# Kernel optimization log

Measured on AMD Instinct MI355X. Metric: run time of the kernel, lower is better.

The kernel has to match this reference:

```python
import jax, jax.numpy as jnp
import numpy as np

NS, NG, NV = 16, 8, 8          # scalar, gate, vector(l=1) multiplicities
CIN = 8                        # input irreps: 8x0
COUT1 = NS + NG + 3 * NV       # 48 channels into gate
CMID = NS + 3 * NV             # 40 channels after gate
KS = 3                         # kernel size
NB = 4                         # radial basis count
P = KS ** 3
BN_EPS = 1e-5

EPS3 = (jnp.zeros((3, 3, 3))
        .at[0, 1, 2].set(1.).at[1, 2, 0].set(1.).at[2, 0, 1].set(1.)
        .at[0, 2, 1].set(-1.).at[2, 1, 0].set(-1.).at[1, 0, 2].set(-1.))


def _lattice():
    c = jnp.linspace(-1., 1., KS)
    g = jnp.stack(jnp.meshgrid(c, c, c, indexing='ij'), -1).reshape(-1, 3)  # [P,3]
    r = jnp.linalg.norm(g, axis=-1)
    rhat = jnp.where(r[:, None] > 0., g / jnp.maximum(r, 1e-9)[:, None], 0.)
    sh0 = jnp.ones_like(r)             # Y_0, component normalization
    sh1 = jnp.sqrt(3.) * rhat          # Y_1, component normalization
    # soft_one_hot_linspace(r, 0, 1, NB, 'smooth_finite', cutoff=False)
    centers = jnp.linspace(0., 1., NB)
    step = centers[1] - centers[0]
    d = (r[:, None] - centers[None, :]) / step
    emb = jnp.where(jnp.abs(d) < 1.,
                    1.14136 * jnp.exp(2.) * jnp.exp(-1. / jnp.maximum(1. - d ** 2, 1e-9)),
                    0.)
    return sh0, sh1, emb


def _kernel1(w1, emb, sh0, sh1):
    # per-lattice-point tensor-product weights: 8x0 (x) (0+1) -> 16x0 + 8x0 + 8x1
    W = (emb @ w1) / KS ** 1.5                 # [P, 256]
    w_ss = W[:, :128].reshape(P, CIN, NS)
    w_sg = W[:, 128:192].reshape(P, CIN, NG)
    w_sv = W[:, 192:256].reshape(P, CIN, NV)
    a = 1. / jnp.sqrt(8.)                      # fan-in per output irrep
    Km = jnp.zeros((P, CIN, COUT1))
    Km = Km.at[:, :, :NS].set(a * w_ss * sh0[:, None, None])
    Km = Km.at[:, :, NS:NS + NG].set(a * w_sg * sh0[:, None, None])
    kv = a * jnp.einsum('pij,pm->pijm', w_sv, sh1)
    return Km.at[:, :, NS + NG:].set(kv.reshape(P, CIN, 3 * NV))


def _kernel2(w2, emb, sh0, sh1):
    # (16x0 + 8x1) (x) (0+1) -> 16x0 + 8x0 + 8x1 with l<=1 CG paths
    W = (emb @ w2) / KS ** 1.5                 # [P, 832]
    w_ss = W[:, 0:256].reshape(P, NS, NS)
    w_sg = W[:, 256:384].reshape(P, NS, NG)
    w_sv = W[:, 384:512].reshape(P, NS, NV)
    w_vv0 = W[:, 512:576].reshape(P, NV, NV)
    w_vs = W[:, 576:704].reshape(P, NV, NS)
    w_vg = W[:, 704:768].reshape(P, NV, NG)
    w_vv1 = W[:, 768:832].reshape(P, NV, NV)
    a_s = 1. / jnp.sqrt(16. + 8.)
    a_v = 1. / jnp.sqrt(16. + 8. + 8.)
    Km = jnp.zeros((P, CMID, COUT1))
    Km = Km.at[:, :NS, :NS].set(a_s * w_ss * sh0[:, None, None])
    Km = Km.at[:, :NS, NS:NS + NG].set(a_s * w_sg * sh0[:, None, None])
    Km = Km.at[:, :NS, NS + NG:].set(
        (a_v * jnp.einsum('pij,pm->pijm', w_sv, sh1)).reshape(P, NS, 3 * NV))
    ks = (a_s / jnp.sqrt(3.)) * jnp.einsum('puj,pm->pumj', w_vs, sh1)
    kg = (a_s / jnp.sqrt(3.)) * jnp.einsum('puj,pm->pumj', w_vg, sh1)
    kv0 = a_v * jnp.einsum('puj,p,mn->pumjn', w_vv0, sh0, jnp.eye(3))
    kv1 = (a_v / jnp.sqrt(6.)) * jnp.einsum('puj,msn,ps->pumjn', w_vv1, EPS3, sh1)
    Km = Km.at[:, NS:, :NS].set(ks.reshape(P, 3 * NV, NS))
    Km = Km.at[:, NS:, NS:NS + NG].set(kg.reshape(P, 3 * NV, NG))
    return Km.at[:, NS:, NS + NG:].set((kv0 + kv1).reshape(P, 3 * NV, 3 * NV))


def _conv3d(x, Km, cin):
    ker = Km.reshape(KS, KS, KS, cin, COUT1).transpose(4, 3, 0, 1, 2)  # [O,I,k,k,k]
    return jax.lax.conv_general_dilated(
        x, ker, (1, 1, 1), 'SAME',
        dimension_numbers=('NCDHW', 'OIDHW', 'NCDHW'))


def _batchnorm(x, ws, bs, wv):
    # e3nn BatchNorm, training statistics, reduce='mean'; x channel-last [...,48]
    s = x[..., :NS + NG]
    mu = s.mean(axis=(0, 1, 2, 3))
    s = s - mu
    var = (s ** 2).mean(axis=(0, 1, 2, 3))
    s = s / jnp.sqrt(var + BN_EPS) * ws + bs
    v = x[..., NS + NG:].reshape(x.shape[:-1] + (NV, 3))
    n2 = (v ** 2).sum(-1).mean(axis=(0, 1, 2, 3))   # [NV]
    v = v * (((n2 + BN_EPS) ** -0.5) * wv)[:, None]
    return jnp.concatenate([s, v.reshape(x.shape[:-1] + (3 * NV,))], -1)


def _gate(x):
    # Gate: relu on scalars, sigmoid gates multiply l=1 fields
    s = jax.nn.relu(x[..., :NS])
    g = jax.nn.sigmoid(x[..., NS:NS + NG])
    v = x[..., NS + NG:].reshape(x.shape[:-1] + (NV, 3)) * g[..., None]
    return jnp.concatenate([s, v.reshape(x.shape[:-1] + (3 * NV,))], -1)


def _forward(x, w1, sc1, w2, sc2_s, sc2_v,
             bn1_ws, bn1_bs, bn1_wv, bn2_ws, bn2_bs, bn2_wv):
    sh0, sh1, emb = _lattice()
    y = _conv3d(x, _kernel1(w1, emb, sh0, sh1), CIN)
    y = y.at[:, :NS + NG].add(
        jnp.einsum('bixyz,io->boxyz', x, sc1) / jnp.sqrt(8.))  # self-connection
    y = jnp.moveaxis(y, 1, -1)
    y = _gate(_batchnorm(y, bn1_ws, bn1_bs, bn1_wv))           # dropout p=0: identity
    y = jnp.moveaxis(y, -1, 1)                                 # [B, 40, X, Y, Z]
    z = _conv3d(y, _kernel2(w2, emb, sh0, sh1), CMID)
    z = z.at[:, :NS + NG].add(
        jnp.einsum('bixyz,io->boxyz', y[:, :NS], sc2_s) / jnp.sqrt(16.))
    yv = y[:, NS:].reshape(y.shape[0], NV, 3, *y.shape[2:])
    scv = jnp.einsum('bumxyz,uj->bjmxyz', yv, sc2_v) / jnp.sqrt(8.)
    z = z.at[:, NS + NG:].add(scv.reshape(z.shape[0], 3 * NV, *z.shape[2:]))
    z = jnp.moveaxis(z, 1, -1)
    z = _gate(_batchnorm(z, bn2_ws, bn2_bs, bn2_wv))
    return jnp.moveaxis(z, -1, 1)                              # [B, 40, X, Y, Z]


def setup_inputs() -> dict:
    key = jax.random.key(0)
    ks = jax.random.split(key, 8)
    B, S = 1, 64
    return {
        'x': jax.random.normal(ks[0], (B, CIN, S, S, S), jnp.float32),
        'w1': jax.random.normal(ks[1], (NB, 256), jnp.float32),
        'sc1': jax.random.normal(ks[2], (CIN, NS + NG), jnp.float32),
        'w2': jax.random.normal(ks[3], (NB, 832), jnp.float32),
        'sc2_s': jax.random.normal(ks[4], (NS, NS + NG), jnp.float32),
        'sc2_v': jax.random.normal(ks[5], (NV, NV), jnp.float32),
        'bn1_ws': jnp.ones((NS + NG,), jnp.float32),
        'bn1_bs': jnp.zeros((NS + NG,), jnp.float32),
        'bn1_wv': jnp.ones((NV,), jnp.float32),
        'bn2_ws': jnp.ones((NS + NG,), jnp.float32),
        'bn2_bs': jnp.zeros((NS + NG,), jnp.float32),
        'bn2_wv': jnp.ones((NV,), jnp.float32),
    }


def reference(x, w1, sc1, w2, sc2_s, sc2_v,
              bn1_ws, bn1_bs, bn1_wv, bn2_ws, bn2_bs, bn2_wv):
    return _forward(x, w1, sc1, w2, sc2_s, sc2_v,
                    bn1_ws, bn1_bs, bn1_wv, bn2_ws, bn2_bs, bn2_wv)
```

## Files before the change

kernel.cpp:

```cpp
#include <hip/hip_runtime.h>
#include <math.h>

#define N3 262144


#define TBL_TOTAL 1728

__device__ inline void lattice_emb(int p, float* embr) {
    int i = p / 9, j = (p / 3) % 3, k = p % 3;
    float gx = (float)(i - 1), gy = (float)(j - 1), gz = (float)(k - 1);
    float r = sqrtf(gx * gx + gy * gy + gz * gz);
    const float centers[4] = {0.f, 0.33333334f, 0.6666667f, 1.f};
    const float step = 0.33333334f;
    #pragma unroll
    for (int b = 0; b < 4; b++) {
        float dd = (r - centers[b]) / step;
        float e = 0.f;
        if (fabsf(dd) < 1.f)
            e = 1.14136f * expf(2.f) * expf(-1.f / fmaxf(1.f - dd * dd, 1e-9f));
        embr[b] = e;
    }
}

__global__ __launch_bounds__(256) void build_tables_kernel(
        const float* __restrict__ w1,  const float* __restrict__ sc1,
        const float* __restrict__ w2,  const float* __restrict__ sc2s,
        const float* __restrict__ sc2v, float* __restrict__ T,
        float* __restrict__ stats1, float* __restrict__ stats2) {
    int gid = blockIdx.x * 256 + threadIdx.x;
    if (gid >= TBL_TOTAL) {
        int r = gid - TBL_TOTAL;
        if (r < 72) stats1[r] = 0.f;
        else if (r < 144) stats2[r - 72] = 0.f;
        return;
    }

    const float inv_ks15 = 0.19245008972987526f;
    const float s3   = 1.7320508075688772f;
    const float a1   = 0.35355339059327373f;
    const float a_s  = 0.2041241452319315f;
    const float a_v  = 0.17677669529663687f;
    const float a_s3 = 0.11785113019775793f;
    const float a_v6 = 0.07216878364870322f;

    float embC[4], embF[4];
    lattice_emb(13, embC);
    lattice_emb(22, embF);

    auto WC1 = [&](int c) { float s=0.f;
        #pragma unroll
        for (int b=0;b<4;b++) s += embC[b]*w1[b*256+c]; return s*inv_ks15; };
    auto WF1 = [&](int c) { float s=0.f;
        #pragma unroll
        for (int b=0;b<4;b++) s += embF[b]*w1[b*256+c]; return s*inv_ks15; };
    auto WC2 = [&](int c) { float s=0.f;
        #pragma unroll
        for (int b=0;b<4;b++) s += embC[b]*w2[b*832+c]; return s*inv_ks15; };
    auto WF2 = [&](int c) { float s=0.f;
        #pragma unroll
        for (int b=0;b<4;b++) s += embF[b]*w2[b*832+c]; return s*inv_ks15; };

    float val = 0.f;
    if (gid < 192) {
        int i = gid / 24, o = gid % 24;
        int c = (o < 16) ? i * 16 + o : 128 + i * 8 + (o - 16);
        val = a1 * WC1(c) + a1 * sc1[i * 24 + o];
    } else if (gid < 384) {
        int r = gid - 192; int i = r / 24, o = r % 24;
        int c = (o < 16) ? i * 16 + o : 128 + i * 8 + (o - 16);
        val = a1 * WF1(c);
    } else if (gid < 448) {
        int r = gid - 384; int i = r / 8, jj = r % 8;
        val = a1 * s3 * WF1(192 + i * 8 + jj);
    } else if (gid < 832) {
        int r = gid - 448; int i = r / 24, o = r % 24;
        int c = (o < 16) ? i * 16 + o : 256 + i * 8 + (o - 16);
        val = a_s * WC2(c) + 0.25f * sc2s[i * 24 + o];
    } else if (gid < 1216) {
        int r = gid - 832; int i = r / 24, o = r % 24;
        int c = (o < 16) ? i * 16 + o : 256 + i * 8 + (o - 16);
        val = a_s * WF2(c);
    } else if (gid < 1344) {
        int r = gid - 1216; int i = r / 8, jj = r % 8;
        val = a_v * s3 * WF2(384 + i * 8 + jj);
    } else if (gid < 1536) {
        int r = gid - 1344; int u = r / 24, o = r % 24;
        int c = (o < 16) ? 576 + u * 16 + o : 704 + u * 8 + (o - 16);
        val = a_s3 * s3 * WF2(c);
    } else if (gid < 1600) {
        int r = gid - 1536; int u = r / 8, jj = r % 8;
        val = a_v * WC2(512 + u * 8 + jj) + a1 * sc2v[u * 8 + jj];
    } else if (gid < 1664) {
        int r = gid - 1600; int u = r / 8, jj = r % 8;
        val = a_v * WF2(512 + u * 8 + jj);
    } else {
        int r = gid - 1664; int u = r / 8, jj = r % 8;
        val = a_v6 * s3 * WF2(768 + u * 8 + jj);
    }
    T[gid] = val;
}

__device__ inline float4 f4z() { return make_float4(0.f, 0.f, 0.f, 0.f); }
__device__ inline float4 f4add(float4 a, float4 b) {
    return make_float4(a.x+b.x, a.y+b.y, a.z+b.z, a.w+b.w); }
__device__ inline float4 f4sub(float4 a, float4 b) {
    return make_float4(a.x-b.x, a.y-b.y, a.z-b.z, a.w-b.w); }
__device__ inline float4 f4fma(float s, float4 a, float4 c) {
    return make_float4(fmaf(s,a.x,c.x), fmaf(s,a.y,c.y), fmaf(s,a.z,c.z), fmaf(s,a.w,c.w)); }
__device__ inline float f4sum(float4 a) { return a.x+a.y+a.z+a.w; }
__device__ inline float f4dot(float4 a) { return a.x*a.x+a.y*a.y+a.z*a.z+a.w*a.w; }

#define LQ5(BP, C_, DM_, DP_, HM_, HP_)                                       \
    {                                                                         \
        const float* _p = (BP);                                               \
        C_  = *(const float4*)_p;                                             \
        DM_ = dmok ? *(const float4*)(_p - 4096) : f4z();                     \
        DP_ = dpok ? *(const float4*)(_p + 4096) : f4z();                     \
        HM_ = hmok ? *(const float4*)(_p -   64) : f4z();                     \
        HP_ = hpok ? *(const float4*)(_p +   64) : f4z();                     \
    }

#define WQ(C_, WM_, WP_)                                                      \
    {                                                                         \
        float _lw = __shfl_up((C_).w, 1, 64);                                 \
        float _rw = __shfl_down((C_).x, 1, 64);                               \
        WM_ = make_float4(wL ? 0.f : _lw, (C_).x, (C_).y, (C_).z);            \
        WP_ = make_float4((C_).y, (C_).z, (C_).w, wR ? 0.f : _rw);            \
    }

__global__ __launch_bounds__(256, 2) void conv1_kernel(const float* __restrict__ x,
                                                       const float* __restrict__ Tg,
                                                       float* __restrict__ out,
                                                       float* __restrict__ stats) {
    __shared__ float T[448];
    __shared__ float red[4][48];
    for (int t = threadIdx.x; t < 448; t += 256) T[t] = Tg[t];
    __syncthreads();

    const int ohalf = blockIdx.y;
    int idx = blockIdx.x * 1024 + threadIdx.x * 4;
    int w0 = idx & 63, h = (idx >> 6) & 63, d = idx >> 12;
    bool dmok = d > 0, dpok = d < 63, hmok = h > 0, hpok = h < 63;
    bool wL = (w0 == 0), wR = (w0 == 60);

    float4 acc[24];
    #pragma unroll
    for (int o = 0; o < 24; o++) acc[o] = f4z();

    float4 nc, ndm, ndp, nhm, nhp;
    LQ5(x + idx, nc, ndm, ndp, nhm, nhp);

    if (ohalf == 0) {
        #pragma unroll 1
        for (int i = 0; i < 8; i++) {
            float4 c = nc, dmq = ndm, dpq = ndp, hmq = nhm, hpq = nhp;
            if (i < 7) LQ5(x + (i + 1) * N3 + idx, nc, ndm, ndp, nhm, nhp);
            float4 wmq, wpq; WQ(c, wmq, wpq);
            float4 S = f4add(f4add(f4add(dmq, dpq), f4add(hmq, hpq)), f4add(wmq, wpq));
            const float* tc = &T[i * 24];
            const float* tf = &T[192 + i * 24];
            #pragma unroll
            for (int o = 0; o < 24; o++)
                acc[o] = f4fma(tc[o], c, f4fma(tf[o], S, acc[o]));
        }
    } else {
        #pragma unroll 1
        for (int i = 0; i < 8; i++) {
            float4 c = nc, dmq = ndm, dpq = ndp, hmq = nhm, hpq = nhp;
            if (i < 7) LQ5(x + (i + 1) * N3 + idx, nc, ndm, ndp, nhm, nhp);
            float4 wmq, wpq; WQ(c, wmq, wpq);
            float4 Dd = f4sub(dpq, dmq), Dh = f4sub(hpq, hmq), Dw = f4sub(wpq, wmq);
            const float* tv = &T[384 + i * 8];
            #pragma unroll
            for (int jj = 0; jj < 8; jj++) {
                float wv = tv[jj];
                acc[jj * 3 + 0] = f4fma(wv, Dd, acc[jj * 3 + 0]);
                acc[jj * 3 + 1] = f4fma(wv, Dh, acc[jj * 3 + 1]);
                acc[jj * 3 + 2] = f4fma(wv, Dw, acc[jj * 3 + 2]);
            }
        }
    }

    int obase = ohalf * 24;
    #pragma unroll
    for (int o = 0; o < 24; o++)
        *(float4*)(out + (obase + o) * N3 + idx) = acc[o];

    int lane = threadIdx.x & 63, wvx = threadIdx.x >> 6;
    if (ohalf == 0) {
        #pragma unroll
        for (int q = 0; q < 48; q++) {
            float val = (q < 24) ? f4sum(acc[q]) : f4dot(acc[q - 24]);
            #pragma unroll
            for (int mq = 32; mq >= 1; mq >>= 1) val += __shfl_xor(val, mq, 64);
            if (lane == 0) red[wvx][q] = val;
        }
        __syncthreads();
        if (threadIdx.x < 48)
            atomicAdd(&stats[threadIdx.x],
                      red[0][threadIdx.x] + red[1][threadIdx.x] +
                      red[2][threadIdx.x] + red[3][threadIdx.x]);
    } else {
        #pragma unroll
        for (int q = 0; q < 24; q++) {
            float val = f4dot(acc[q]);
            #pragma unroll
            for (int mq = 32; mq >= 1; mq >>= 1) val += __shfl_xor(val, mq, 64);
            if (lane == 0) red[wvx][q] = val;
        }
        __syncthreads();
        if (threadIdx.x < 24)
            atomicAdd(&stats[48 + threadIdx.x],
                      red[0][threadIdx.x] + red[1][threadIdx.x] +
                      red[2][threadIdx.x] + red[3][threadIdx.x]);
    }
}

__global__ __launch_bounds__(256, 2) void conv2_kernel(const float* __restrict__ y,
                                                       const float* __restrict__ Tg,
                                                       float* __restrict__ out,
                                                       float* __restrict__ stats) {
    __shared__ float T[1280];
    __shared__ float red[4][48];
    for (int t = threadIdx.x; t < 1280; t += 256) T[t] = Tg[448 + t];
    __syncthreads();

    const int ohalf = blockIdx.y;
    int idx = blockIdx.x * 1024 + threadIdx.x * 4;
    int w0 = idx & 63, h = (idx >> 6) & 63, d = idx >> 12;
    bool dmok = d > 0, dpok = d < 63, hmok = h > 0, hpok = h < 63;
    bool wL = (w0 == 0), wR = (w0 == 60);

    float4 acc[24];
    #pragma unroll
    for (int o = 0; o < 24; o++) acc[o] = f4z();

    if (ohalf == 0) {
        float4 nc, ndm, ndp, nhm, nhp;
        LQ5(y + idx, nc, ndm, ndp, nhm, nhp);
        #pragma unroll 1
        for (int i = 0; i < 16; i++) {
            float4 c = nc, dmq = ndm, dpq = ndp, hmq = nhm, hpq = nhp;
            if (i < 15) LQ5(y + (i + 1) * N3 + idx, nc, ndm, ndp, nhm, nhp);
            float4 wmq, wpq; WQ(c, wmq, wpq);
            float4 S = f4add(f4add(f4add(dmq, dpq), f4add(hmq, hpq)), f4add(wmq, wpq));
            const float* tc = &T[i * 24];
            const float* tf = &T[384 + i * 24];
            #pragma unroll
            for (int o = 0; o < 24; o++)
                acc[o] = f4fma(tc[o], c, f4fma(tf[o], S, acc[o]));
        }
        #pragma unroll 1
        for (int u = 0; u < 8; u++) {
            const float* b0 = y + (16 + u * 3) * N3 + idx;
            float4 qdm = dmok ? *(const float4*)(b0 - 4096) : f4z();
            float4 qdp = dpok ? *(const float4*)(b0 + 4096) : f4z();
            float4 qhm = hmok ? *(const float4*)(b0 + N3 - 64) : f4z();
            float4 qhp = hpok ? *(const float4*)(b0 + N3 + 64) : f4z();
            float4 c2  = *(const float4*)(b0 + 2 * N3);
            float4 wmq, wpq; WQ(c2, wmq, wpq);
            float4 Dsum = f4add(f4add(f4sub(qdp, qdm), f4sub(qhp, qhm)), f4sub(wpq, wmq));
            const float* tvs = &T[896 + u * 24];
            #pragma unroll
            for (int o = 0; o < 24; o++)
                acc[o] = f4fma(tvs[o], Dsum, acc[o]);
        }
    } else {
        float4 nc, ndm, ndp, nhm, nhp;
        LQ5(y + idx, nc, ndm, ndp, nhm, nhp);
        #pragma unroll 1
        for (int i = 0; i < 16; i++) {
            float4 c = nc, dmq = ndm, dpq = ndp, hmq = nhm, hpq = nhp;
            if (i < 15) LQ5(y + (i + 1) * N3 + idx, nc, ndm, ndp, nhm, nhp);
            float4 wmq, wpq; WQ(c, wmq, wpq);
            float4 Dd = f4sub(dpq, dmq), Dh = f4sub(hpq, hmq), Dw = f4sub(wpq, wmq);
            const float* tv = &T[768 + i * 8];
            #pragma unroll
            for (int jj = 0; jj < 8; jj++) {
                float wv = tv[jj];
                acc[jj * 3 + 0] = f4fma(wv, Dd, acc[jj * 3 + 0]);
                acc[jj * 3 + 1] = f4fma(wv, Dh, acc[jj * 3 + 1]);
                acc[jj * 3 + 2] = f4fma(wv, Dw, acc[jj * 3 + 2]);
            }
        }
        #pragma unroll 1
        for (int u = 0; u < 8; u++) {
            const float* t0c = &T[1088 + u * 8];
            const float* t0f = &T[1152 + u * 8];
            const float* tv1 = &T[1216 + u * 8];
            {
                float4 c, dmq, dpq, hmq, hpq;
                LQ5(y + (16 + u * 3 + 0) * N3 + idx, c, dmq, dpq, hmq, hpq);
                float4 wmq, wpq; WQ(c, wmq, wpq);
                float4 S = f4add(f4add(f4add(dmq, dpq), f4add(hmq, hpq)), f4add(wmq, wpq));
                float4 Dh = f4sub(hpq, hmq), Dw = f4sub(wpq, wmq);
                #pragma unroll
                for (int jj = 0; jj < 8; jj++) {
                    float k1 = tv1[jj];
                    acc[jj * 3 + 0] = f4fma(t0c[jj], c, f4fma(t0f[jj], S, acc[jj * 3 + 0]));
                    acc[jj * 3 + 2] = f4fma(k1, Dh, acc[jj * 3 + 2]);
                    acc[jj * 3 + 1] = f4fma(-k1, Dw, acc[jj * 3 + 1]);
                }
            }
            {
                float4 c, dmq, dpq, hmq, hpq;
                LQ5(y + (16 + u * 3 + 1) * N3 + idx, c, dmq, dpq, hmq, hpq);
                float4 wmq, wpq; WQ(c, wmq, wpq);
                float4 S = f4add(f4add(f4add(dmq, dpq), f4add(hmq, hpq)), f4add(wmq, wpq));
                float4 Dd = f4sub(dpq, dmq), Dw = f4sub(wpq, wmq);
                #pragma unroll
                for (int jj = 0; jj < 8; jj++) {
                    float k1 = tv1[jj];
                    acc[jj * 3 + 1] = f4fma(t0c[jj], c, f4fma(t0f[jj], S, acc[jj * 3 + 1]));
                    acc[jj * 3 + 0] = f4fma(k1, Dw, acc[jj * 3 + 0]);
                    acc[jj * 3 + 2] = f4fma(-k1, Dd, acc[jj * 3 + 2]);
                }
            }
            {
                float4 c, dmq, dpq, hmq, hpq;
                LQ5(y + (16 + u * 3 + 2) * N3 + idx, c, dmq, dpq, hmq, hpq);
                float4 wmq, wpq; WQ(c, wmq, wpq);
                float4 S = f4add(f4add(f4add(dmq, dpq), f4add(hmq, hpq)), f4add(wmq, wpq));
                float4 Dd = f4sub(dpq, dmq), Dh = f4sub(hpq, hmq);
                #pragma unroll
                for (int jj = 0; jj < 8; jj++) {
                    float k1 = tv1[jj];
                    acc[jj * 3 + 2] = f4fma(t0c[jj], c, f4fma(t0f[jj], S, acc[jj * 3 + 2]));
                    acc[jj * 3 + 1] = f4fma(k1, Dd, acc[jj * 3 + 1]);
                    acc[jj * 3 + 0] = f4fma(-k1, Dh, acc[jj * 3 + 0]);
                }
            }
        }
    }

    int obase = ohalf * 24;
    #pragma unroll
    for (int o = 0; o < 24; o++)
        *(float4*)(out + (obase + o) * N3 + idx) = acc[o];

    int lane = threadIdx.x & 63, wvx = threadIdx.x >> 6;
    if (ohalf == 0) {
        #pragma unroll
        for (int q = 0; q < 48; q++) {
            float val = (q < 24) ? f4sum(acc[q]) : f4dot(acc[q - 24]);
            #pragma unroll
            for (int mq = 32; mq >= 1; mq >>= 1) val += __shfl_xor(val, mq, 64);
            if (lane == 0) red[wvx][q] = val;
        }
        __syncthreads();
        if (threadIdx.x < 48)
            atomicAdd(&stats[threadIdx.x],
                      red[0][threadIdx.x] + red[1][threadIdx.x] +
                      red[2][threadIdx.x] + red[3][threadIdx.x]);
    } else {
        #pragma unroll
        for (int q = 0; q < 24; q++) {
            float val = f4dot(acc[q]);
            #pragma unroll
            for (int mq = 32; mq >= 1; mq >>= 1) val += __shfl_xor(val, mq, 64);
            if (lane == 0) red[wvx][q] = val;
        }
        __syncthreads();
        if (threadIdx.x < 24)
            atomicAdd(&stats[48 + threadIdx.x],
                      red[0][threadIdx.x] + red[1][threadIdx.x] +
                      red[2][threadIdx.x] + red[3][threadIdx.x]);
    }
}

__global__ __launch_bounds__(256) void bn_gate_kernel(const float* __restrict__ zp,
                                                      const float* __restrict__ stats,
                                                      const float* __restrict__ wsc,
                                                      const float* __restrict__ bsc,
                                                      const float* __restrict__ wvc,
                                                      float* __restrict__ out) {
    __shared__ float sb[56];
    if (threadIdx.x < 32) {
        int t = threadIdx.x;
        const float invN = 1.0f / 262144.0f;
        if (t < 24) {
            float mu = stats[t] * invN;
            float var = stats[24 + t] * invN - mu * mu;
            float inv = rsqrtf(var + 1e-5f);
            sb[t] = wsc[t] * inv;
            sb[24 + t] = bsc[t] - mu * wsc[t] * inv;
        } else {
            int u = t - 24;
            float s2 = stats[48 + u * 3] + stats[48 + u * 3 + 1] + stats[48 + u * 3 + 2];
            sb[48 + u] = wvc[u] * rsqrtf(s2 * invN + 1e-5f);
        }
    }
    __syncthreads();

    int idx = (blockIdx.x * 256 + threadIdx.x) * 2;
    float2 g[8];
    #pragma unroll
    for (int u = 0; u < 8; u++) {
        float2 v = *(const float2*)(zp + (16 + u) * N3 + idx);
        float sc = sb[16 + u], bi = sb[40 + u];
        g[u].x = 1.0f / (1.0f + expf(-(v.x * sc + bi)));
        g[u].y = 1.0f / (1.0f + expf(-(v.y * sc + bi)));
    }
    #pragma unroll
    for (int c = 0; c < 16; c++) {
        float2 v = *(const float2*)(zp + c * N3 + idx);
        float sc = sb[c], bi = sb[24 + c];
        float2 r;
        r.x = fmaxf(v.x * sc + bi, 0.f);
        r.y = fmaxf(v.y * sc + bi, 0.f);
        *(float2*)(out + c * N3 + idx) = r;
    }
    #pragma unroll
    for (int u = 0; u < 8; u++) {
        float sv = sb[48 + u];
        #pragma unroll
        for (int m = 0; m < 3; m++) {
            float2 v = *(const float2*)(zp + (24 + u * 3 + m) * N3 + idx);
            float2 r;
            r.x = v.x * sv * g[u].x;
            r.y = v.y * sv * g[u].y;
            *(float2*)(out + (16 + u * 3 + m) * N3 + idx) = r;
        }
    }
}

extern "C" void kernel_launch(void* const* d_in, const int* in_sizes, int n_in,
                              void* d_out, int out_size, void* d_ws, size_t ws_size,
                              hipStream_t stream) {
    const float* x      = (const float*)d_in[0];
    const float* w1     = (const float*)d_in[1];
    const float* sc1    = (const float*)d_in[2];
    const float* w2     = (const float*)d_in[3];
    const float* sc2s   = (const float*)d_in[4];
    const float* sc2v   = (const float*)d_in[5];
    const float* bn1_ws = (const float*)d_in[6];
    const float* bn1_bs = (const float*)d_in[7];
    const float* bn1_wv = (const float*)d_in[8];
    const float* bn2_ws = (const float*)d_in[9];
    const float* bn2_bs = (const float*)d_in[10];
    const float* bn2_wv = (const float*)d_in[11];
    float* out = (float*)d_out;
    char* ws = (char*)d_ws;

    float* Tg     = (float*)(ws + 0);
    float* stats1 = (float*)(ws + 8192);
    float* stats2 = (float*)(ws + 8192 + 512);
    float* bufA   = (float*)(ws + 262144);

    hipLaunchKernelGGL(build_tables_kernel, dim3(8), dim3(256), 0, stream,
                       w1, sc1, w2, sc2s, sc2v, Tg, stats1, stats2);
    hipLaunchKernelGGL(conv1_kernel, dim3(256, 2), dim3(256), 0, stream, x, Tg, bufA, stats1);
    hipLaunchKernelGGL(bn_gate_kernel, dim3(512), dim3(256), 0, stream,
                       bufA, stats1, bn1_ws, bn1_bs, bn1_wv, out);
    hipLaunchKernelGGL(conv2_kernel, dim3(256, 2), dim3(256), 0, stream, out, Tg, bufA, stats2);
    hipLaunchKernelGGL(bn_gate_kernel, dim3(512), dim3(256), 0, stream,
                       bufA, stats2, bn2_ws, bn2_bs, bn2_wv, out);
}
```

Measured before the change: 111.1 us.

## Fuse conv and BN-gate stages via cooperative grid sync, keep accumulators in registers

Each convolution is merged with its batch-norm and gate step into one cooperative kernel. After accumulating, each block publishes its channel statistics, waits at a grid-wide barrier, then applies normalization, ReLU and sigmoid gating straight from its register accumulators. Only the 8 gate channels go through a scratch buffer, because the vector-half blocks need them. This removes the round trip of the full 48-channel pre-normalization tensor through global memory and drops two kernel launches. In exchange it adds a grid barrier and depends on all 512 blocks being resident at once, with a fallback to the old separate kernels if the cooperative launch fails.

```diff
diff --git a/kernel.cpp b/kernel.cpp
--- a/kernel.cpp
+++ b/kernel.cpp
@@ -1,5 +1,8 @@
 #include <hip/hip_runtime.h>
+#include <hip/hip_cooperative_groups.h>
 #include <math.h>
+
+namespace cg = cooperative_groups;
 
 #define N3 262144
 
@@ -109,6 +112,7 @@
     return make_float4(fmaf(s,a.x,c.x), fmaf(s,a.y,c.y), fmaf(s,a.z,c.z), fmaf(s,a.w,c.w)); }
 __device__ inline float f4sum(float4 a) { return a.x+a.y+a.z+a.w; }
 __device__ inline float f4dot(float4 a) { return a.x*a.x+a.y*a.y+a.z*a.z+a.w*a.w; }
+__device__ inline float sigm(float v) { return 1.0f / (1.0f + expf(-v)); }
 
 #define LQ5(BP, C_, DM_, DP_, HM_, HP_)                                       \
     {                                                                         \
@@ -128,244 +132,270 @@
         WP_ = make_float4((C_).y, (C_).z, (C_).w, wR ? 0.f : _rw);            \
     }
 
-__global__ __launch_bounds__(256, 2) void conv1_kernel(const float* __restrict__ x,
-                                                       const float* __restrict__ Tg,
-                                                       float* __restrict__ out,
-                                                       float* __restrict__ stats) {
+#define CONV1_BODY(SRC)                                                       \
+    {                                                                         \
+        float4 nc, ndm, ndp, nhm, nhp;                                        \
+        LQ5((SRC) + idx, nc, ndm, ndp, nhm, nhp);                             \
+        if (ohalf == 0) {                                                     \
+            _Pragma("unroll 1")                                               \
+            for (int i = 0; i < 8; i++) {                                     \
+                float4 c = nc, dmq = ndm, dpq = ndp, hmq = nhm, hpq = nhp;    \
+                if (i < 7) LQ5((SRC) + (i + 1) * N3 + idx, nc, ndm, ndp, nhm, nhp); \
+                float4 wmq, wpq; WQ(c, wmq, wpq);                             \
+                float4 S = f4add(f4add(f4add(dmq, dpq), f4add(hmq, hpq)), f4add(wmq, wpq)); \
+                const float* tc = &T[i * 24];                                 \
+                const float* tf = &T[192 + i * 24];                           \
+                _Pragma("unroll")                                             \
+                for (int o = 0; o < 24; o++)                                  \
+                    acc[o] = f4fma(tc[o], c, f4fma(tf[o], S, acc[o]));        \
+            }                                                                 \
+        } else {                                                              \
+            _Pragma("unroll 1")                                               \
+            for (int i = 0; i < 8; i++) {                                     \
+                float4 c = nc, dmq = ndm, dpq = ndp, hmq = nhm, hpq = nhp;    \
+                if (i < 7) LQ5((SRC) + (i + 1) * N3 + idx, nc, ndm, ndp, nhm, nhp); \
+                float4 wmq, wpq; WQ(c, wmq, wpq);                             \
+                float4 Dd = f4sub(dpq, dmq), Dh = f4sub(hpq, hmq), Dw = f4sub(wpq, wmq); \
+                const float* tv = &T[384 + i * 8];                            \
+                _Pragma("unroll")                                             \
+                for (int jj = 0; jj < 8; jj++) {                              \
+                    float wv = tv[jj];                                        \
+                    acc[jj * 3 + 0] = f4fma(wv, Dd, acc[jj * 3 + 0]);         \
+                    acc[jj * 3 + 1] = f4fma(wv, Dh, acc[jj * 3 + 1]);         \
+                    acc[jj * 3 + 2] = f4fma(wv, Dw, acc[jj * 3 + 2]);         \
+                }                                                             \
+            }                                                                 \
+        }                                                                     \
+    }
+
+#define CONV2_BODY(SRC)                                                       \
+    if (ohalf == 0) {                                                         \
+        float4 nc, ndm, ndp, nhm, nhp;                                        \
+        LQ5((SRC) + idx, nc, ndm, ndp, nhm, nhp);                             \
+        _Pragma("unroll 1")                                                   \
+        for (int i = 0; i < 16; i++) {                                        \
+            float4 c = nc, dmq = ndm, dpq = ndp, hmq = nhm, hpq = nhp;        \
+            if (i < 15) LQ5((SRC) + (i + 1) * N3 + idx, nc, ndm, ndp, nhm, nhp); \
+            float4 wmq, wpq; WQ(c, wmq, wpq);                                 \
+            float4 S = f4add(f4add(f4add(dmq, dpq), f4add(hmq, hpq)), f4add(wmq, wpq)); \
+            const float* tc = &T[i * 24];                                     \
+            const float* tf = &T[384 + i * 24];                               \
+            _Pragma("unroll")                                                 \
+            for (int o = 0; o < 24; o++)                                      \
+                acc[o] = f4fma(tc[o], c, f4fma(tf[o], S, acc[o]));            \
+        }                                                                     \
+        _Pragma("unroll 1")                                                   \
+        for (int u = 0; u < 8; u++) {                                         \
+            const float* b0 = (SRC) + (16 + u * 3) * N3 + idx;                \
+            float4 qdm = dmok ? *(const float4*)(b0 - 4096) : f4z();          \
+            float4 qdp = dpok ? *(const float4*)(b0 + 4096) : f4z();          \
+            float4 qhm = hmok ? *(const float4*)(b0 + N3 - 64) : f4z();       \
+            float4 qhp = hpok ? *(const float4*)(b0 + N3 + 64) : f4z();       \
+            float4 c2  = *(const float4*)(b0 + 2 * N3);                       \
+            float4 wmq, wpq; WQ(c2, wmq, wpq);                                \
+            float4 Dsum = f4add(f4add(f4sub(qdp, qdm), f4sub(qhp, qhm)), f4sub(wpq, wmq)); \
+            const float* tvs = &T[896 + u * 24];                              \
+            _Pragma("unroll")                                                 \
+            for (int o = 0; o < 24; o++)                                      \
+                acc[o] = f4fma(tvs[o], Dsum, acc[o]);                         \
+        }                                                                     \
+    } else {                                                                  \
+        float4 nc, ndm, ndp, nhm, nhp;                                        \
+        LQ5((SRC) + idx, nc, ndm, ndp, nhm, nhp);                             \
+        _Pragma("unroll 1")                                                   \
+        for (int i = 0; i < 16; i++) {                                        \
+            float4 c = nc, dmq = ndm, dpq = ndp, hmq = nhm, hpq = nhp;        \
+            if (i < 15) LQ5((SRC) + (i + 1) * N3 + idx, nc, ndm, ndp, nhm, nhp); \
+            float4 wmq, wpq; WQ(c, wmq, wpq);                                 \
+            float4 Dd = f4sub(dpq, dmq), Dh = f4sub(hpq, hmq), Dw = f4sub(wpq, wmq); \
+            const float* tv = &T[768 + i * 8];                                \
+            _Pragma("unroll")                                                 \
+            for (int jj = 0; jj < 8; jj++) {                                  \
+                float wv = tv[jj];                                            \
+                acc[jj * 3 + 0] = f4fma(wv, Dd, acc[jj * 3 + 0]);             \
+                acc[jj * 3 + 1] = f4fma(wv, Dh, acc[jj * 3 + 1]);             \
+                acc[jj * 3 + 2] = f4fma(wv, Dw, acc[jj * 3 + 2]);             \
+            }                                                                 \
+        }                                                                     \
+        _Pragma("unroll 1")                                                   \
+        for (int u = 0; u < 8; u++) {                                         \
+            const float* t0c = &T[1088 + u * 8];                              \
+            const float* t0f = &T[1152 + u * 8];                              \
+            const float* tv1 = &T[1216 + u * 8];                              \
+            {                                                                 \
+                float4 c, dmq, dpq, hmq, hpq;                                 \
+                LQ5((SRC) + (16 + u * 3 + 0) * N3 + idx, c, dmq, dpq, hmq, hpq); \
+                float4 wmq, wpq; WQ(c, wmq, wpq);                             \
+                float4 S = f4add(f4add(f4add(dmq, dpq), f4add(hmq, hpq)), f4add(wmq, wpq)); \
+                float4 Dh = f4sub(hpq, hmq), Dw = f4sub(wpq, wmq);            \
+                _Pragma("unroll")                                             \
+                for (int jj = 0; jj < 8; jj++) {                              \
+                    float k1 = tv1[jj];                                       \
+                    acc[jj * 3 + 0] = f4fma(t0c[jj], c, f4fma(t0f[jj], S, acc[jj * 3 + 0])); \
+                    acc[jj * 3 + 2] = f4fma(k1, Dh, acc[jj * 3 + 2]);         \
+                    acc[jj * 3 + 1] = f4fma(-k1, Dw, acc[jj * 3 + 1]);        \
+                }                                                             \
+            }                                                                 \
+            {                                                                 \
+                float4 c, dmq, dpq, hmq, hpq;                                 \
+                LQ5((SRC) + (16 + u * 3 + 1) * N3 + idx, c, dmq, dpq, hmq, hpq); \
+                float4 wmq, wpq; WQ(c, wmq, wpq);                             \
+                float4 S = f4add(f4add(f4add(dmq, dpq), f4add(hmq, hpq)), f4add(wmq, wpq)); \
+                float4 Dd = f4sub(dpq, dmq), Dw = f4sub(wpq, wmq);            \
+                _Pragma("unroll")                                             \
+                for (int jj = 0; jj < 8; jj++) {                              \
+                    float k1 = tv1[jj];                                       \
+                    acc[jj * 3 + 1] = f4fma(t0c[jj], c, f4fma(t0f[jj], S, acc[jj * 3 + 1])); \
+                    acc[jj * 3 + 0] = f4fma(k1, Dw, acc[jj * 3 + 0]);         \
+                    acc[jj * 3 + 2] = f4fma(-k1, Dd, acc[jj * 3 + 2]);        \
+                }                                                             \
+            }                                                                 \
+            {                                                                 \
+                float4 c, dmq, dpq, hmq, hpq;                                 \
+                LQ5((SRC) + (16 + u * 3 + 2) * N3 + idx, c, dmq, dpq, hmq, hpq); \
+                float4 wmq, wpq; WQ(c, wmq, wpq);                             \
+                float4 S = f4add(f4add(f4add(dmq, dpq), f4add(hmq, hpq)), f4add(wmq, wpq)); \
+                float4 Dd = f4sub(dpq, dmq), Dh = f4sub(hpq, hmq);            \
+                _Pragma("unroll")                                             \
+                for (int jj = 0; jj < 8; jj++) {                              \
+                    float k1 = tv1[jj];                                       \
+                    acc[jj * 3 + 2] = f4fma(t0c[jj], c, f4fma(t0f[jj], S, acc[jj * 3 + 2])); \
+                    acc[jj * 3 + 1] = f4fma(k1, Dd, acc[jj * 3 + 1]);         \
+                    acc[jj * 3 + 0] = f4fma(-k1, Dh, acc[jj * 3 + 0]);        \
+                }                                                             \
+            }                                                                 \
+        }                                                                     \
+    }
+
+#define STATS_REDUCE(STATS)                                                   \
+    {                                                                         \
+        int lane = threadIdx.x & 63, wvx = threadIdx.x >> 6;                  \
+        if (ohalf == 0) {                                                     \
+            _Pragma("unroll")                                                 \
+            for (int q = 0; q < 48; q++) {                                    \
+                float val = (q < 24) ? f4sum(acc[q]) : f4dot(acc[q - 24]);    \
+                _Pragma("unroll")                                             \
+                for (int mq = 32; mq >= 1; mq >>= 1) val += __shfl_xor(val, mq, 64); \
+                if (lane == 0) red[wvx][q] = val;                             \
+            }                                                                 \
+            __syncthreads();                                                  \
+            if (threadIdx.x < 48)                                             \
+                atomicAdd(&(STATS)[threadIdx.x],                              \
+                          red[0][threadIdx.x] + red[1][threadIdx.x] +         \
+                          red[2][threadIdx.x] + red[3][threadIdx.x]);         \
+        } else {                                                              \
+            _Pragma("unroll")                                                 \
+            for (int q = 0; q < 24; q++) {                                    \
+                float val = f4dot(acc[q]);                                    \
+                _Pragma("unroll")                                             \
+                for (int mq = 32; mq >= 1; mq >>= 1) val += __shfl_xor(val, mq, 64); \
+                if (lane == 0) red[wvx][q] = val;                             \
+            }                                                                 \
+            __syncthreads();                                                  \
+            if (threadIdx.x < 24)                                             \
+                atomicAdd(&(STATS)[48 + threadIdx.x],                         \
+                          red[0][threadIdx.x] + red[1][threadIdx.x] +         \
+                          red[2][threadIdx.x] + red[3][threadIdx.x]);         \
+        }                                                                     \
+    }
+
+#define FINALIZE_SB(STATS, WSC, BSC, WVC)                                     \
+    if (threadIdx.x < 32) {                                                   \
+        int t = threadIdx.x;                                                  \
+        const float invN = 1.0f / 262144.0f;                                  \
+        if (t < 24) {                                                         \
+            float mu = (STATS)[t] * invN;                                     \
+            float var = (STATS)[24 + t] * invN - mu * mu;                     \
+            float inv = rsqrtf(var + 1e-5f);                                  \
+            sb[t] = (WSC)[t] * inv;                                           \
+            sb[24 + t] = (BSC)[t] - mu * (WSC)[t] * inv;                      \
+        } else {                                                              \
+            int u = t - 24;                                                   \
+            float s2 = (STATS)[48 + u * 3] + (STATS)[48 + u * 3 + 1] +        \
+                       (STATS)[48 + u * 3 + 2];                               \
+            sb[48 + u] = (WVC)[u] * rsqrtf(s2 * invN + 1e-5f);                \
+        }                                                                     \
+    }                                                                         \
+    __syncthreads();
+
+#define GATED_EPILOGUE(DST, GBUF)                                             \
+    if (ohalf == 0) {                                                         \
+        _Pragma("unroll")                                                     \
+        for (int c = 0; c < 16; c++) {                                        \
+            float4 v = acc[c];                                                \
+            float scl = sb[c], bi = sb[24 + c];                               \
+            float4 r;                                                         \
+            r.x = fmaxf(v.x * scl + bi, 0.f);                                 \
+            r.y = fmaxf(v.y * scl + bi, 0.f);                                 \
+            r.z = fmaxf(v.z * scl + bi, 0.f);                                 \
+            r.w = fmaxf(v.w * scl + bi, 0.f);                                 \
+            *(float4*)((DST) + c * N3 + idx) = r;                             \
+        }                                                                     \
+    } else {                                                                  \
+        _Pragma("unroll 1")                                                   \
+        for (int u = 0; u < 8; u++) {                                         \
+            float4 gv = *(const float4*)((GBUF) + u * N3 + idx);              \
+            float scl = sb[16 + u], bi = sb[40 + u], sv = sb[48 + u];         \
+            float4 g;                                                         \
+            g.x = sigm(gv.x * scl + bi) * sv;                                 \
+            g.y = sigm(gv.y * scl + bi) * sv;                                 \
+            g.z = sigm(gv.z * scl + bi) * sv;                                 \
+            g.w = sigm(gv.w * scl + bi) * sv;                                 \
+            _Pragma("unroll")                                                 \
+            for (int m = 0; m < 3; m++) {                                     \
+                float4 a = acc[u * 3 + m];                                    \
+                float4 r = make_float4(a.x * g.x, a.y * g.y, a.z * g.z, a.w * g.w); \
+                *(float4*)((DST) + (16 + u * 3 + m) * N3 + idx) = r;          \
+            }                                                                 \
+        }                                                                     \
+    }
+
+__global__ __launch_bounds__(256, 2) void conv1_plain(const float* __restrict__ x,
+                                                      const float* __restrict__ Tg,
+                                                      float* __restrict__ out,
+                                                      float* __restrict__ stats) {
     __shared__ float T[448];
     __shared__ float red[4][48];
     for (int t = threadIdx.x; t < 448; t += 256) T[t] = Tg[t];
     __syncthreads();
-
     const int ohalf = blockIdx.y;
     int idx = blockIdx.x * 1024 + threadIdx.x * 4;
     int w0 = idx & 63, h = (idx >> 6) & 63, d = idx >> 12;
     bool dmok = d > 0, dpok = d < 63, hmok = h > 0, hpok = h < 63;
     bool wL = (w0 == 0), wR = (w0 == 60);
-
     float4 acc[24];
     #pragma unroll
     for (int o = 0; o < 24; o++) acc[o] = f4z();
-
-    float4 nc, ndm, ndp, nhm, nhp;
-    LQ5(x + idx, nc, ndm, ndp, nhm, nhp);
-
-    if (ohalf == 0) {
-        #pragma unroll 1
-        for (int i = 0; i < 8; i++) {
-            float4 c = nc, dmq = ndm, dpq = ndp, hmq = nhm, hpq = nhp;
-            if (i < 7) LQ5(x + (i + 1) * N3 + idx, nc, ndm, ndp, nhm, nhp);
-            float4 wmq, wpq; WQ(c, wmq, wpq);
-            float4 S = f4add(f4add(f4add(dmq, dpq), f4add(hmq, hpq)), f4add(wmq, wpq));
-            const float* tc = &T[i * 24];
-            const float* tf = &T[192 + i * 24];
-            #pragma unroll
-            for (int o = 0; o < 24; o++)
-                acc[o] = f4fma(tc[o], c, f4fma(tf[o], S, acc[o]));
-        }
-    } else {
-        #pragma unroll 1
-        for (int i = 0; i < 8; i++) {
-            float4 c = nc, dmq = ndm, dpq = ndp, hmq = nhm, hpq = nhp;
-            if (i < 7) LQ5(x + (i + 1) * N3 + idx, nc, ndm, ndp, nhm, nhp);
-            float4 wmq, wpq; WQ(c, wmq, wpq);
-            float4 Dd = f4sub(dpq, dmq), Dh = f4sub(hpq, hmq), Dw = f4sub(wpq, wmq);
-            const float* tv = &T[384 + i * 8];
-            #pragma unroll
-            for (int jj = 0; jj < 8; jj++) {
-                float wv = tv[jj];
-                acc[jj * 3 + 0] = f4fma(wv, Dd, acc[jj * 3 + 0]);
-                acc[jj * 3 + 1] = f4fma(wv, Dh, acc[jj * 3 + 1]);
-                acc[jj * 3 + 2] = f4fma(wv, Dw, acc[jj * 3 + 2]);
-            }
-        }
-    }
-
+    CONV1_BODY(x);
     int obase = ohalf * 24;
     #pragma unroll
     for (int o = 0; o < 24; o++)
         *(float4*)(out + (obase + o) * N3 + idx) = acc[o];
-
-    int lane = threadIdx.x & 63, wvx = threadIdx.x >> 6;
-    if (ohalf == 0) {
-        #pragma unroll
-        for (int q = 0; q < 48; q++) {
-            float val = (q < 24) ? f4sum(acc[q]) : f4dot(acc[q - 24]);
-            #pragma unroll
-            for (int mq = 32; mq >= 1; mq >>= 1) val += __shfl_xor(val, mq, 64);
-            if (lane == 0) red[wvx][q] = val;
-        }
-        __syncthreads();
-        if (threadIdx.x < 48)
-            atomicAdd(&stats[threadIdx.x],
-                      red[0][threadIdx.x] + red[1][threadIdx.x] +
-                      red[2][threadIdx.x] + red[3][threadIdx.x]);
-    } else {
-        #pragma unroll
-        for (int q = 0; q < 24; q++) {
-            float val = f4dot(acc[q]);
-            #pragma unroll
-            for (int mq = 32; mq >= 1; mq >>= 1) val += __shfl_xor(val, mq, 64);
-            if (lane == 0) red[wvx][q] = val;
-        }
-        __syncthreads();
-        if (threadIdx.x < 24)
-            atomicAdd(&stats[48 + threadIdx.x],
-                      red[0][threadIdx.x] + red[1][threadIdx.x] +
-                      red[2][threadIdx.x] + red[3][threadIdx.x]);
-    }
-}
-
-__global__ __launch_bounds__(256, 2) void conv2_kernel(const float* __restrict__ y,
-                                                       const float* __restrict__ Tg,
-                                                       float* __restrict__ out,
-                                                       float* __restrict__ stats) {
+    STATS_REDUCE(stats);
+}
+
+__global__ __launch_bounds__(256, 2) void conv2_plain(const float* __restrict__ y,
+                                                      const float* __restrict__ Tg,
+                                                      float* __restrict__ out,
+                                                      float* __restrict__ stats) {
     __shared__ float T[1280];
     __shared__ float red[4][48];
     for (int t = threadIdx.x; t < 1280; t += 256) T[t] = Tg[448 + t];
     __syncthreads();
-
     const int ohalf = blockIdx.y;
     int idx = blockIdx.x * 1024 + threadIdx.x * 4;
     int w0 = idx & 63, h = (idx >> 6) & 63, d = idx >> 12;
     bool dmok = d > 0, dpok = d < 63, hmok = h > 0, hpok = h < 63;
     bool wL = (w0 == 0), wR = (w0 == 60);
-
     float4 acc[24];
     #pragma unroll
     for (int o = 0; o < 24; o++) acc[o] = f4z();
-
-    if (ohalf == 0) {
-        float4 nc, ndm, ndp, nhm, nhp;
-        LQ5(y + idx, nc, ndm, ndp, nhm, nhp);
-        #pragma unroll 1
-        for (int i = 0; i < 16; i++) {
-            float4 c = nc, dmq = ndm, dpq = ndp, hmq = nhm, hpq = nhp;
-            if (i < 15) LQ5(y + (i + 1) * N3 + idx, nc, ndm, ndp, nhm, nhp);
-            float4 wmq, wpq; WQ(c, wmq, wpq);
-            float4 S = f4add(f4add(f4add(dmq, dpq), f4add(hmq, hpq)), f4add(wmq, wpq));
-            const float* tc = &T[i * 24];
-            const float* tf = &T[384 + i * 24];
-            #pragma unroll
-            for (int o = 0; o < 24; o++)
-                acc[o] = f4fma(tc[o], c, f4fma(tf[o], S, acc[o]));
-        }
-        #pragma unroll 1
-        for (int u = 0; u < 8; u++) {
-            const float* b0 = y + (16 + u * 3) * N3 + idx;
-            float4 qdm = dmok ? *(const float4*)(b0 - 4096) : f4z();
-            float4 qdp = dpok ? *(const float4*)(b0 + 4096) : f4z();
-            float4 qhm = hmok ? *(const float4*)(b0 + N3 - 64) : f4z();
-            float4 qhp = hpok ? *(const float4*)(b0 + N3 + 64) : f4z();
-            float4 c2  = *(const float4*)(b0 + 2 * N3);
-            float4 wmq, wpq; WQ(c2, wmq, wpq);
-            float4 Dsum = f4add(f4add(f4sub(qdp, qdm), f4sub(qhp, qhm)), f4sub(wpq, wmq));
-            const float* tvs = &T[896 + u * 24];
-            #pragma unroll
-            for (int o = 0; o < 24; o++)
-                acc[o] = f4fma(tvs[o], Dsum, acc[o]);
-        }
-    } else {
-        float4 nc, ndm, ndp, nhm, nhp;
-        LQ5(y + idx, nc, ndm, ndp, nhm, nhp);
-        #pragma unroll 1
-        for (int i = 0; i < 16; i++) {
-            float4 c = nc, dmq = ndm, dpq = ndp, hmq = nhm, hpq = nhp;
-            if (i < 15) LQ5(y + (i + 1) * N3 + idx, nc, ndm, ndp, nhm, nhp);
-            float4 wmq, wpq; WQ(c, wmq, wpq);
-            float4 Dd = f4sub(dpq, dmq), Dh = f4sub(hpq, hmq), Dw = f4sub(wpq, wmq);
-            const float* tv = &T[768 + i * 8];
-            #pragma unroll
-            for (int jj = 0; jj < 8; jj++) {
-                float wv = tv[jj];
-                acc[jj * 3 + 0] = f4fma(wv, Dd, acc[jj * 3 + 0]);
-                acc[jj * 3 + 1] = f4fma(wv, Dh, acc[jj * 3 + 1]);
-                acc[jj * 3 + 2] = f4fma(wv, Dw, acc[jj * 3 + 2]);
-            }
-        }
-        #pragma unroll 1
-        for (int u = 0; u < 8; u++) {
-            const float* t0c = &T[1088 + u * 8];
-            const float* t0f = &T[1152 + u * 8];
-            const float* tv1 = &T[1216 + u * 8];
-            {
-                float4 c, dmq, dpq, hmq, hpq;
-                LQ5(y + (16 + u * 3 + 0) * N3 + idx, c, dmq, dpq, hmq, hpq);
-                float4 wmq, wpq; WQ(c, wmq, wpq);
-                float4 S = f4add(f4add(f4add(dmq, dpq), f4add(hmq, hpq)), f4add(wmq, wpq));
-                float4 Dh = f4sub(hpq, hmq), Dw = f4sub(wpq, wmq);
-                #pragma unroll
-                for (int jj = 0; jj < 8; jj++) {
-                    float k1 = tv1[jj];
-                    acc[jj * 3 + 0] = f4fma(t0c[jj], c, f4fma(t0f[jj], S, acc[jj * 3 + 0]));
-                    acc[jj * 3 + 2] = f4fma(k1, Dh, acc[jj * 3 + 2]);
-                    acc[jj * 3 + 1] = f4fma(-k1, Dw, acc[jj * 3 + 1]);
-                }
-            }
-            {
-                float4 c, dmq, dpq, hmq, hpq;
-                LQ5(y + (16 + u * 3 + 1) * N3 + idx, c, dmq, dpq, hmq, hpq);
-                float4 wmq, wpq; WQ(c, wmq, wpq);
-                float4 S = f4add(f4add(f4add(dmq, dpq), f4add(hmq, hpq)), f4add(wmq, wpq));
-                float4 Dd = f4sub(dpq, dmq), Dw = f4sub(wpq, wmq);
-                #pragma unroll
-                for (int jj = 0; jj < 8; jj++) {
-                    float k1 = tv1[jj];
-                    acc[jj * 3 + 1] = f4fma(t0c[jj], c, f4fma(t0f[jj], S, acc[jj * 3 + 1]));
-                    acc[jj * 3 + 0] = f4fma(k1, Dw, acc[jj * 3 + 0]);
-                    acc[jj * 3 + 2] = f4fma(-k1, Dd, acc[jj * 3 + 2]);
-                }
-            }
-            {
-                float4 c, dmq, dpq, hmq, hpq;
-                LQ5(y + (16 + u * 3 + 2) * N3 + idx, c, dmq, dpq, hmq, hpq);
-                float4 wmq, wpq; WQ(c, wmq, wpq);
-                float4 S = f4add(f4add(f4add(dmq, dpq), f4add(hmq, hpq)), f4add(wmq, wpq));
-                float4 Dd = f4sub(dpq, dmq), Dh = f4sub(hpq, hmq);
-                #pragma unroll
-                for (int jj = 0; jj < 8; jj++) {
-                    float k1 = tv1[jj];
-                    acc[jj * 3 + 2] = f4fma(t0c[jj], c, f4fma(t0f[jj], S, acc[jj * 3 + 2]));
-                    acc[jj * 3 + 1] = f4fma(k1, Dd, acc[jj * 3 + 1]);
-                    acc[jj * 3 + 0] = f4fma(-k1, Dh, acc[jj * 3 + 0]);
-                }
-            }
-        }
-    }
-
+    CONV2_BODY(y);
     int obase = ohalf * 24;
     #pragma unroll
     for (int o = 0; o < 24; o++)
         *(float4*)(out + (obase + o) * N3 + idx) = acc[o];
-
-    int lane = threadIdx.x & 63, wvx = threadIdx.x >> 6;
-    if (ohalf == 0) {
-        #pragma unroll
-        for (int q = 0; q < 48; q++) {
-            float val = (q < 24) ? f4sum(acc[q]) : f4dot(acc[q - 24]);
-            #pragma unroll
-            for (int mq = 32; mq >= 1; mq >>= 1) val += __shfl_xor(val, mq, 64);
-            if (lane == 0) red[wvx][q] = val;
-        }
-        __syncthreads();
-        if (threadIdx.x < 48)
-            atomicAdd(&stats[threadIdx.x],
-                      red[0][threadIdx.x] + red[1][threadIdx.x] +
-                      red[2][threadIdx.x] + red[3][threadIdx.x]);
-    } else {
-        #pragma unroll
-        for (int q = 0; q < 24; q++) {
-            float val = f4dot(acc[q]);
-            #pragma unroll
-            for (int mq = 32; mq >= 1; mq >>= 1) val += __shfl_xor(val, mq, 64);
-            if (lane == 0) red[wvx][q] = val;
-        }
-        __syncthreads();
-        if (threadIdx.x < 24)
-            atomicAdd(&stats[48 + threadIdx.x],
-                      red[0][threadIdx.x] + red[1][threadIdx.x] +
-                      red[2][threadIdx.x] + red[3][threadIdx.x]);
-    }
+    STATS_REDUCE(stats);
 }
 
 __global__ __launch_bounds__(256) void bn_gate_kernel(const float* __restrict__ zp,
@@ -375,22 +405,7 @@
                                                       const float* __restrict__ wvc,
                                                       float* __restrict__ out) {
     __shared__ float sb[56];
-    if (threadIdx.x < 32) {
-        int t = threadIdx.x;
-        const float invN = 1.0f / 262144.0f;
-        if (t < 24) {
-            float mu = stats[t] * invN;
-            float var = stats[24 + t] * invN - mu * mu;
-            float inv = rsqrtf(var + 1e-5f);
-            sb[t] = wsc[t] * inv;
-            sb[24 + t] = bsc[t] - mu * wsc[t] * inv;
-        } else {
-            int u = t - 24;
-            float s2 = stats[48 + u * 3] + stats[48 + u * 3 + 1] + stats[48 + u * 3 + 2];
-            sb[48 + u] = wvc[u] * rsqrtf(s2 * invN + 1e-5f);
-        }
-    }
-    __syncthreads();
+    FINALIZE_SB(stats, wsc, bsc, wvc);
 
     int idx = (blockIdx.x * 256 + threadIdx.x) * 2;
     float2 g[8];
@@ -398,8 +413,8 @@
     for (int u = 0; u < 8; u++) {
         float2 v = *(const float2*)(zp + (16 + u) * N3 + idx);
         float sc = sb[16 + u], bi = sb[40 + u];
-        g[u].x = 1.0f / (1.0f + expf(-(v.x * sc + bi)));
-        g[u].y = 1.0f / (1.0f + expf(-(v.y * sc + bi)));
+        g[u].x = sigm(v.x * sc + bi);
+        g[u].y = sigm(v.y * sc + bi);
     }
     #pragma unroll
     for (int c = 0; c < 16; c++) {
@@ -422,6 +437,82 @@
             *(float2*)(out + (16 + u * 3 + m) * N3 + idx) = r;
         }
     }
+}
+
+__global__ __launch_bounds__(256, 2) void conv1_fused(
+        const float* __restrict__ x, const float* __restrict__ Tg,
+        float* __restrict__ y, float* __restrict__ gbuf,
+        float* __restrict__ stats,
+        const float* __restrict__ wsc, const float* __restrict__ bsc,
+        const float* __restrict__ wvc) {
+    __shared__ float T[448];
+    __shared__ float red[4][48];
+    __shared__ float sb[56];
+    for (int t = threadIdx.x; t < 448; t += 256) T[t] = Tg[t];
+    __syncthreads();
+
+    const int bid = blockIdx.x;
+    const int ohalf = bid >> 8;
+    int idx = (bid & 255) * 1024 + threadIdx.x * 4;
+    int w0 = idx & 63, h = (idx >> 6) & 63, d = idx >> 12;
+    bool dmok = d > 0, dpok = d < 63, hmok = h > 0, hpok = h < 63;
+    bool wL = (w0 == 0), wR = (w0 == 60);
+
+    float4 acc[24];
+    #pragma unroll
+    for (int o = 0; o < 24; o++) acc[o] = f4z();
+    CONV1_BODY(x);
+
+    if (ohalf == 0) {
+        #pragma unroll
+        for (int u = 0; u < 8; u++)
+            *(float4*)(gbuf + u * N3 + idx) = acc[16 + u];
+    }
+    STATS_REDUCE(stats);
+
+    __threadfence();
+    cg::this_grid().sync();
+
+    FINALIZE_SB(stats, wsc, bsc, wvc);
+    GATED_EPILOGUE(y, gbuf);
+}
+
+__global__ __launch_bounds__(256, 2) void conv2_fused(
+        const float* __restrict__ y, const float* __restrict__ Tg,
+        float* __restrict__ out, float* __restrict__ gbuf,
+        float* __restrict__ stats,
+        const float* __restrict__ wsc, const float* __restrict__ bsc,
+        const float* __restrict__ wvc) {
+    __shared__ float T[1280];
+    __shared__ float red[4][48];
+    __shared__ float sb[56];
+    for (int t = threadIdx.x; t < 1280; t += 256) T[t] = Tg[448 + t];
+    __syncthreads();
+
+    const int bid = blockIdx.x;
+    const int ohalf = bid >> 8;
+    int idx = (bid & 255) * 1024 + threadIdx.x * 4;
+    int w0 = idx & 63, h = (idx >> 6) & 63, d = idx >> 12;
+    bool dmok = d > 0, dpok = d < 63, hmok = h > 0, hpok = h < 63;
+    bool wL = (w0 == 0), wR = (w0 == 60);
+
+    float4 acc[24];
+    #pragma unroll
+    for (int o = 0; o < 24; o++) acc[o] = f4z();
+    CONV2_BODY(y);
+
+    if (ohalf == 0) {
+        #pragma unroll
+        for (int u = 0; u < 8; u++)
+            *(float4*)(gbuf + u * N3 + idx) = acc[16 + u];
+    }
+    STATS_REDUCE(stats);
+
+    __threadfence();
+    cg::this_grid().sync();
+
+    FINALIZE_SB(stats, wsc, bsc, wvc);
+    GATED_EPILOGUE(out, gbuf);
 }
 
 extern "C" void kernel_launch(void* const* d_in, const int* in_sizes, int n_in,
@@ -445,14 +536,38 @@
     float* Tg     = (float*)(ws + 0);
     float* stats1 = (float*)(ws + 8192);
     float* stats2 = (float*)(ws + 8192 + 512);
-    float* bufA   = (float*)(ws + 262144);
+    float* zbuf   = (float*)(ws + 262144);
+    float* gbuf   = zbuf;
 
     hipLaunchKernelGGL(build_tables_kernel, dim3(8), dim3(256), 0, stream,
                        w1, sc1, w2, sc2s, sc2v, Tg, stats1, stats2);
-    hipLaunchKernelGGL(conv1_kernel, dim3(256, 2), dim3(256), 0, stream, x, Tg, bufA, stats1);
-    hipLaunchKernelGGL(bn_gate_kernel, dim3(512), dim3(256), 0, stream,
-                       bufA, stats1, bn1_ws, bn1_bs, bn1_wv, out);
-    hipLaunchKernelGGL(conv2_kernel, dim3(256, 2), dim3(256), 0, stream, out, Tg, bufA, stats2);
-    hipLaunchKernelGGL(bn_gate_kernel, dim3(512), dim3(256), 0, stream,
-                       bufA, stats2, bn2_ws, bn2_bs, bn2_wv, out);
-}
+
+    {
+        void* args[] = {(void*)&x, (void*)&Tg, (void*)&out, (void*)&gbuf,
+                        (void*)&stats1, (void*)&bn1_ws, (void*)&bn1_bs, (void*)&bn1_wv};
+        hipError_t e = hipLaunchCooperativeKernel((const void*)conv1_fused,
+                                                  dim3(512), dim3(256), args, 0, stream);
+        if (e != hipSuccess) {
+            (void)hipGetLastError();
+            hipLaunchKernelGGL(conv1_plain, dim3(256, 2), dim3(256), 0, stream,
+                               x, Tg, zbuf, stats1);
+            hipLaunchKernelGGL(bn_gate_kernel, dim3(512), dim3(256), 0, stream,
+                               zbuf, stats1, bn1_ws, bn1_bs, bn1_wv, out);
+        }
+    }
+
+    {
+        const float* yin = (const float*)out;
+        void* args[] = {(void*)&yin, (void*)&Tg, (void*)&out, (void*)&gbuf,
+                        (void*)&stats2, (void*)&bn2_ws, (void*)&bn2_bs, (void*)&bn2_wv};
+        hipError_t e = hipLaunchCooperativeKernel((const void*)conv2_fused,
+                                                  dim3(512), dim3(256), args, 0, stream);
+        if (e != hipSuccess) {
+            (void)hipGetLastError();
+            hipLaunchKernelGGL(conv2_plain, dim3(256, 2), dim3(256), 0, stream,
+                               out, Tg, zbuf, stats2);
+            hipLaunchKernelGGL(bn_gate_kernel, dim3(512), dim3(256), 0, stream,
+                               zbuf, stats2, bn2_ws, bn2_bs, bn2_wv, out);
+        }
+    }
+}
```

Result: slower. 426.6 us (+283.9%).
